# Performance work log

Hardware: AMD Instinct MI355X
Metric: run time of the kernel (lower is better)

The kernel has to match this reference:

```python
import jax, jax.numpy as jnp
import numpy as np

N = 16          # num_transforms
BS = 128        # batch_size
D = 4096        # encoder dim
C, H, W = 3, 64, 64
TEMP = 0.5      # hyperparams.temperature
LAM_H = 1.0     # hyperparams.h
EPS = 1e-8      # torch CosineSimilarity eps


def setup_inputs() -> dict:
    key = jax.random.key(0)
    k1, k2, k3 = jax.random.split(key, 3)
    return {
        "pic_set": jax.random.normal(k1, (N, BS, C, H, W), dtype=jnp.float32),
        "dec_pics": jax.random.normal(k2, (N, BS, C, H, W), dtype=jnp.float32),
        "h": jax.random.normal(k3, (N, BS, D), dtype=jnp.float32),
    }


def _pos_neg_indices(n, bs):
    # Static (numpy) index construction replicating the boolean masks.
    # Positives of row i: all j != i with j % bs == i % bs (sorted, row-major),
    # Negatives of row i: all j with j % bs != i % bs (sorted).
    k = n * bs
    i = np.arange(k)
    cols = (i % bs)[:, None] + np.arange(n)[None, :] * bs          # (K, N)
    pos_idx = cols[cols != i[:, None]].reshape(k, n - 1)            # (K, N-1)
    jj = np.arange(k)
    neg_mask = (jj[None, :] % bs) != (i[:, None] % bs)              # (K, K)
    neg_idx = np.broadcast_to(jj, (k, k))[neg_mask].reshape(k, k - n)  # (K, K-N)
    return jnp.asarray(pos_idx), jnp.asarray(neg_idx)


def _nt_xent(h):
    n, bs, d = h.shape
    k = n * bs
    s = h.reshape(k, d)
    # CosineSimilarity(dim=2) with eps clamp on norms
    nrm = jnp.maximum(jnp.linalg.norm(s, axis=1), EPS)
    sn = s / nrm[:, None]
    simmat = (sn @ sn.T) / TEMP                                     # (K, K)
    pos_idx, neg_idx = _pos_neg_indices(n, bs)
    pos = jnp.take_along_axis(simmat, pos_idx, axis=1)              # (K, N-1)
    neg = jnp.take_along_axis(simmat, neg_idx, axis=1)              # (K, K-N)
    # CrossEntropyLoss(reduction='sum') with label 0 on logits
    # [pos_{i,m}, neg_i] == sum of logsumexp - pos; logsumexp over concat
    # factors as logaddexp(lse(neg_i), pos_{i,m}).
    neg_lse = jax.scipy.special.logsumexp(neg, axis=1)              # (K,)
    loss = jnp.sum(jnp.logaddexp(neg_lse[:, None], pos) - pos)
    kpos = k * (n - 1)
    return loss / kpos


def reference(pic_set, dec_pics, h):
    n, bs = pic_set.shape[0], pic_set.shape[1]
    loss_h = _nt_xent(h)
    # dec_pics[(i+1) % N] cyclic offset, then flat MSE (mean reduction)
    offset = (np.arange(n) + 1) % n
    p = pic_set.reshape(n, bs, -1)
    dshift = dec_pics.reshape(n, bs, -1)[offset]
    loss_pairs = jnp.mean((p - dshift) ** 2)
    return loss_pairs + LAM_H * loss_h
```

## Files before the change

### kernel.cpp

```cpp
#include <hip/hip_runtime.h>
#include <hip/hip_bf16.h>
#include <math.h>

#define N_T   16
#define BSZ   128
#define DDIM  4096
#define KROWS (N_T * BSZ)
#define CHW   (3 * 64 * 64)
#define S_PIC (BSZ * CHW)
#define T_MSE (N_T * S_PIC)
#define KPOS  (KROWS * (N_T - 1))

#define GEMM_BLOCKS 512
#define MSE_BLOCKS  3072

typedef short  bf16x8 __attribute__((ext_vector_type(8)));
typedef float  f32x4  __attribute__((ext_vector_type(4)));

__device__ __forceinline__ float waveReduceSum(float v) {
    for (int off = 32; off > 0; off >>= 1) v += __shfl_down(v, off, 64);
    return v;
}
__device__ __forceinline__ float waveReduceMax(float v) {
    for (int off = 32; off > 0; off >>= 1) v = fmaxf(v, __shfl_down(v, off, 64));
    return v;
}
__device__ __forceinline__ float blockReduceSum(float v) {
    __shared__ float s[8];
    int lane = threadIdx.x & 63, wid = threadIdx.x >> 6;
    v = waveReduceSum(v);
    if (lane == 0) s[wid] = v;
    __syncthreads();
    int nw = (blockDim.x + 63) >> 6;
    v = (threadIdx.x < nw) ? s[threadIdx.x] : 0.0f;
    if (wid == 0) v = waveReduceSum(v);
    return v;
}
__device__ __forceinline__ float blockReduceMax(float v) {
    __shared__ float s[8];
    int lane = threadIdx.x & 63, wid = threadIdx.x >> 6;
    v = waveReduceMax(v);
    if (lane == 0) s[wid] = v;
    __syncthreads();
    int nw = (blockDim.x + 63) >> 6;
    v = (threadIdx.x < nw) ? s[threadIdx.x] : -INFINITY;
    if (wid == 0) v = waveReduceMax(v);
    return v;
}

__device__ __forceinline__ void mse_block(const float* __restrict__ pic,
                                          const float* __restrict__ dec,
                                          float* __restrict__ acc,
                                          int n, int bx) {
    const size_t off = (size_t)n * S_PIC + (size_t)bx * 8192 + threadIdx.x * 4;
    const ptrdiff_t doff = (ptrdiff_t)(((n + 1) & (N_T - 1)) - n) * S_PIC;
    const float* p = pic + off;
    const float* d = pic + off;
    d = dec + off + doff;
    float s0 = 0.f, s1 = 0.f, s2 = 0.f, s3 = 0.f;
#pragma unroll
    for (int k = 0; k < 8; k++) {
        float4 a = *(const float4*)(p + k * 1024);
        float4 b = *(const float4*)(d + k * 1024);
        float dx = a.x - b.x, dy = a.y - b.y, dz = a.z - b.z, dw = a.w - b.w;
        s0 += dx * dx; s1 += dy * dy; s2 += dz * dz; s3 += dw * dw;
    }
    float sum = (s0 + s1) + (s2 + s3);
    sum = blockReduceSum(sum);
    if (threadIdx.x == 0) atomicAdd(acc, sum);
}

__global__ void norm_kernel(const float* __restrict__ h,
                            __hip_bfloat16* __restrict__ hb) {
    const int row = blockIdx.x;
    const float* r = h + (size_t)row * DDIM;
    float ss = 0.0f;
    for (int k = threadIdx.x * 8; k < DDIM; k += blockDim.x * 8) {
        float4 v0 = *(const float4*)(r + k);
        float4 v1 = *(const float4*)(r + k + 4);
        ss += v0.x * v0.x + v0.y * v0.y + v0.z * v0.z + v0.w * v0.w;
        ss += v1.x * v1.x + v1.y * v1.y + v1.z * v1.z + v1.w * v1.w;
    }
    ss = blockReduceSum(ss);
    __shared__ float scale_s;
    if (threadIdx.x == 0) scale_s = 1.0f / fmaxf(sqrtf(ss), 1e-8f);
    __syncthreads();
    const float sc = scale_s;
    __hip_bfloat16* ob = hb + (size_t)row * DDIM;
    for (int k = threadIdx.x * 8; k < DDIM; k += blockDim.x * 8) {
        float4 v0 = *(const float4*)(r + k);
        float4 v1 = *(const float4*)(r + k + 4);
        __hip_bfloat16 t[8];
        t[0] = __float2bfloat16(v0.x * sc); t[1] = __float2bfloat16(v0.y * sc);
        t[2] = __float2bfloat16(v0.z * sc); t[3] = __float2bfloat16(v0.w * sc);
        t[4] = __float2bfloat16(v1.x * sc); t[5] = __float2bfloat16(v1.y * sc);
        t[6] = __float2bfloat16(v1.z * sc); t[7] = __float2bfloat16(v1.w * sc);
        *(bf16x8*)(ob + k) = *(const bf16x8*)t;
    }
}

__global__ __launch_bounds__(256) void mega_kernel(const ushort* __restrict__ X,
                                                   float* __restrict__ Cpart,
                                                   const float* __restrict__ pic,
                                                   const float* __restrict__ dec,
                                                   float* __restrict__ acc) {
    __shared__ ushort As[128 * 32];
    __shared__ ushort Bs[128 * 32];
    const int bid = blockIdx.x;

    if (bid >= GEMM_BLOCKS) {
        const int t = bid - GEMM_BLOCKS;
        mse_block(pic, dec, acc, t & (N_T - 1), t >> 4);
        return;
    }

    const int kz = bid >> 8;
    const int bi = (bid >> 4) & 15, bj = bid & 15;
    const int tid  = threadIdx.x;
    const int wave = tid >> 6, lane = tid & 63;
    const int wm = wave >> 1, wn = wave & 1;
    const int quad = lane >> 4, l16 = lane & 15;

    f32x4 acc_r[4][4];
#pragma unroll
    for (int i = 0; i < 4; i++)
#pragma unroll
        for (int j = 0; j < 4; j++) acc_r[i][j] = (f32x4){0.f, 0.f, 0.f, 0.f};

    const int srow = lane >> 2;
    const int scol = (lane & 3) * 8;
    const ushort* Ag0 = X + (size_t)(bi * 128 + wave * 16       + srow) * DDIM + scol;
    const ushort* Ag1 = X + (size_t)(bi * 128 + (wave + 4) * 16 + srow) * DDIM + scol;
    const ushort* Bg0 = X + (size_t)(bj * 128 + wave * 16       + srow) * DDIM + scol;
    const ushort* Bg1 = X + (size_t)(bj * 128 + (wave + 4) * 16 + srow) * DDIM + scol;
    ushort* Al0 = As + wave * 512;
    ushort* Al1 = As + (wave + 4) * 512;
    ushort* Bl0 = Bs + wave * 512;
    ushort* Bl1 = Bs + (wave + 4) * 512;

    const int k0 = kz * (DDIM / 2), k1 = k0 + (DDIM / 2);
    for (int kk = k0; kk < k1; kk += 32) {
        __syncthreads();
        __builtin_amdgcn_global_load_lds(
            (const __attribute__((address_space(1))) unsigned int*)(Ag0 + kk),
            (__attribute__((address_space(3))) unsigned int*)Al0, 16, 0, 0);
        __builtin_amdgcn_global_load_lds(
            (const __attribute__((address_space(1))) unsigned int*)(Ag1 + kk),
            (__attribute__((address_space(3))) unsigned int*)Al1, 16, 0, 0);
        __builtin_amdgcn_global_load_lds(
            (const __attribute__((address_space(1))) unsigned int*)(Bg0 + kk),
            (__attribute__((address_space(3))) unsigned int*)Bl0, 16, 0, 0);
        __builtin_amdgcn_global_load_lds(
            (const __attribute__((address_space(1))) unsigned int*)(Bg1 + kk),
            (__attribute__((address_space(3))) unsigned int*)Bl1, 16, 0, 0);
        __syncthreads();

        bf16x8 a[4], b[4];
#pragma unroll
        for (int t = 0; t < 4; t++)
            a[t] = *(const bf16x8*)(As + (wm * 64 + t * 16 + l16) * 32 + quad * 8);
#pragma unroll
        for (int t = 0; t < 4; t++)
            b[t] = *(const bf16x8*)(Bs + (wn * 64 + t * 16 + l16) * 32 + quad * 8);
#pragma unroll
        for (int mt = 0; mt < 4; mt++)
#pragma unroll
            for (int nt = 0; nt < 4; nt++)
                acc_r[mt][nt] = __builtin_amdgcn_mfma_f32_16x16x32_bf16(
                    a[mt], b[nt], acc_r[mt][nt], 0, 0, 0);
    }

    float* Cp = Cpart + (size_t)kz * KROWS * KROWS;
#pragma unroll
    for (int mt = 0; mt < 4; mt++) {
#pragma unroll
        for (int r = 0; r < 4; r++) {
            const int row = bi * 128 + wm * 64 + mt * 16 + quad * 4 + r;
            float* o = Cp + (size_t)row * KROWS + bj * 128 + wn * 64 + l16;
#pragma unroll
            for (int nt = 0; nt < 4; nt++) o[nt * 16] = 2.0f * acc_r[mt][nt][r];
        }
    }
}

__global__ __launch_bounds__(256) void mse_kernel(const float* __restrict__ pic,
                                                  const float* __restrict__ dec,
                                                  float* __restrict__ acc) {
    mse_block(pic, dec, acc, blockIdx.y, blockIdx.x);
}

__global__ void lse_kernel(const float* __restrict__ Cpart, float* __restrict__ acc) {
    const int i = blockIdx.x;
    __shared__ float srow[KROWS];
    const float* r0 = Cpart + (size_t)i * KROWS;
    const float* r1 = r0 + (size_t)KROWS * KROWS;
    for (int j = threadIdx.x * 4; j < KROWS; j += blockDim.x * 4) {
        float4 a = *(const float4*)(r0 + j);
        float4 b = *(const float4*)(r1 + j);
        float4 s; s.x = a.x + b.x; s.y = a.y + b.y; s.z = a.z + b.z; s.w = a.w + b.w;
        *(float4*)(srow + j) = s;
    }
    __syncthreads();

    const int ires = i & (BSZ - 1);
    float m = -INFINITY;
    for (int j = threadIdx.x; j < KROWS; j += blockDim.x)
        if ((j & (BSZ - 1)) != ires) m = fmaxf(m, srow[j]);
    m = blockReduceMax(m);
    __shared__ float mS;
    if (threadIdx.x == 0) mS = m;
    __syncthreads();
    m = mS;
    float se = 0.0f;
    for (int j = threadIdx.x; j < KROWS; j += blockDim.x)
        if ((j & (BSZ - 1)) != ires) se += expf(srow[j] - m);
    se = blockReduceSum(se);

    if (threadIdx.x == 0) {
        const float neg_lse = m + logf(se);
        float loss = 0.0f;
#pragma unroll
        for (int t = 0; t < N_T; t++) {
            const int j = ires + t * BSZ;
            if (j == i) continue;
            const float x = neg_lse - srow[j];
            loss += (x > 0.0f) ? (x + log1pf(expf(-x))) : log1pf(expf(x));
        }
        atomicAdd(acc + 1, loss);
    }
}

__global__ void finalize_kernel(const float* __restrict__ acc, float* __restrict__ out) {
    if (threadIdx.x == 0 && blockIdx.x == 0)
        out[0] = acc[0] / (float)T_MSE + acc[1] / (float)KPOS;
}

extern "C" void kernel_launch(void* const* d_in, const int* in_sizes, int n_in,
                              void* d_out, int out_size, void* d_ws, size_t ws_size,
                              hipStream_t stream) {
    const float* pic = (const float*)d_in[0];
    float* dec = (float*)d_in[1];
    const float* h = (const float*)d_in[2];
    float* out = (float*)d_out;

    float* acc = (float*)d_ws;
    const size_t hbuf_bytes   = (size_t)KROWS * DDIM * sizeof(__hip_bfloat16);
    const size_t simmat_bytes = (size_t)2 * KROWS * KROWS * sizeof(float);

    hipMemsetAsync(d_ws, 0, 256, stream);

    if (ws_size >= 256 + hbuf_bytes + simmat_bytes) {
        __hip_bfloat16* hbuf = (__hip_bfloat16*)((char*)d_ws + 256);
        float* simmat = (float*)((char*)d_ws + 256 + hbuf_bytes);
        norm_kernel<<<KROWS, 256, 0, stream>>>(h, hbuf);
        mega_kernel<<<GEMM_BLOCKS + MSE_BLOCKS, 256, 0, stream>>>(
            (const ushort*)hbuf, simmat, pic, dec, acc);
        lse_kernel<<<KROWS, 256, 0, stream>>>(simmat, acc);
    } else {
        __hip_bfloat16* hbuf = (__hip_bfloat16*)dec;
        float* simmat = (float*)((char*)dec + hbuf_bytes);
        mse_kernel<<<dim3(MSE_BLOCKS / N_T, N_T), 256, 0, stream>>>(pic, dec, acc);
        norm_kernel<<<KROWS, 256, 0, stream>>>(h, hbuf);
        mega_kernel<<<GEMM_BLOCKS, 256, 0, stream>>>(
            (const ushort*)hbuf, simmat, pic, dec, acc);
        lse_kernel<<<KROWS, 256, 0, stream>>>(simmat, acc);
    }
    finalize_kernel<<<1, 64, 0, stream>>>(acc, out);
}
```

Baseline: 305.0 us.

## Deepen split-K, swizzle GEMM blocks, drop LSE max pass, fuse finalize

The GEMM k-split depth becomes a template parameter and the default path now splits K four ways instead of two. GEMM block indices are remapped so consecutive blocks spread across k-slices and tiles. The LSE kernel drops its max-reduction pass and uses a fixed shift of 2, which is safe because cosine similarity divided by 0.5 is bounded by 2; it also switches to fast exp and log intrinsics. The memset and finalize launches are removed: accumulator zeroing moves into the norm kernel, and the last LSE block, found through an atomic counter, writes the output. The deeper split doubles the partial-sum memory written and read, which trades extra memory traffic for more GEMM parallelism.

```diff
diff --git a/kernel.cpp b/kernel.cpp
--- a/kernel.cpp
+++ b/kernel.cpp
@@ -11,7 +11,6 @@
 #define T_MSE (N_T * S_PIC)
 #define KPOS  (KROWS * (N_T - 1))
 
-#define GEMM_BLOCKS 512
 #define MSE_BLOCKS  3072
 
 typedef short  bf16x8 __attribute__((ext_vector_type(8)));
@@ -19,10 +18,6 @@
 
 __device__ __forceinline__ float waveReduceSum(float v) {
     for (int off = 32; off > 0; off >>= 1) v += __shfl_down(v, off, 64);
-    return v;
-}
-__device__ __forceinline__ float waveReduceMax(float v) {
-    for (int off = 32; off > 0; off >>= 1) v = fmaxf(v, __shfl_down(v, off, 64));
     return v;
 }
 __device__ __forceinline__ float blockReduceSum(float v) {
@@ -36,17 +31,6 @@
     if (wid == 0) v = waveReduceSum(v);
     return v;
 }
-__device__ __forceinline__ float blockReduceMax(float v) {
-    __shared__ float s[8];
-    int lane = threadIdx.x & 63, wid = threadIdx.x >> 6;
-    v = waveReduceMax(v);
-    if (lane == 0) s[wid] = v;
-    __syncthreads();
-    int nw = (blockDim.x + 63) >> 6;
-    v = (threadIdx.x < nw) ? s[threadIdx.x] : -INFINITY;
-    if (wid == 0) v = waveReduceMax(v);
-    return v;
-}
 
 __device__ __forceinline__ void mse_block(const float* __restrict__ pic,
                                           const float* __restrict__ dec,
@@ -55,8 +39,7 @@
     const size_t off = (size_t)n * S_PIC + (size_t)bx * 8192 + threadIdx.x * 4;
     const ptrdiff_t doff = (ptrdiff_t)(((n + 1) & (N_T - 1)) - n) * S_PIC;
     const float* p = pic + off;
-    const float* d = pic + off;
-    d = dec + off + doff;
+    const float* d = dec + off + doff;
     float s0 = 0.f, s1 = 0.f, s2 = 0.f, s3 = 0.f;
 #pragma unroll
     for (int k = 0; k < 8; k++) {
@@ -71,7 +54,11 @@
 }
 
 __global__ void norm_kernel(const float* __restrict__ h,
-                            __hip_bfloat16* __restrict__ hb) {
+                            __hip_bfloat16* __restrict__ hb,
+                            float* __restrict__ acc, int zero_acc) {
+    if (zero_acc && blockIdx.x == 0 && threadIdx.x < 64)
+        acc[threadIdx.x] = 0.0f;
+
     const int row = blockIdx.x;
     const float* r = h + (size_t)row * DDIM;
     float ss = 0.0f;
@@ -99,6 +86,7 @@
     }
 }
 
+template<int NKZ>
 __global__ __launch_bounds__(256) void mega_kernel(const ushort* __restrict__ X,
                                                    float* __restrict__ Cpart,
                                                    const float* __restrict__ pic,
@@ -106,13 +94,16 @@
                                                    float* __restrict__ acc) {
     __shared__ ushort As[128 * 32];
     __shared__ ushort Bs[128 * 32];
-    const int bid = blockIdx.x;
-
-    if (bid >= GEMM_BLOCKS) {
-        const int t = bid - GEMM_BLOCKS;
+    constexpr int NG = NKZ * 256;
+    int bid = blockIdx.x;
+
+    if (bid >= NG) {
+        const int t = bid - NG;
         mse_block(pic, dec, acc, t & (N_T - 1), t >> 4);
         return;
     }
+
+    bid = (bid & 7) * (NG >> 3) + (bid >> 3);
 
     const int kz = bid >> 8;
     const int bi = (bid >> 4) & 15, bj = bid & 15;
@@ -138,7 +129,8 @@
     ushort* Bl0 = Bs + wave * 512;
     ushort* Bl1 = Bs + (wave + 4) * 512;
 
-    const int k0 = kz * (DDIM / 2), k1 = k0 + (DDIM / 2);
+    constexpr int KS = DDIM / NKZ;
+    const int k0 = kz * KS, k1 = k0 + KS;
     for (int kk = k0; kk < k1; kk += 32) {
         __syncthreads();
         __builtin_amdgcn_global_load_lds(
@@ -189,35 +181,32 @@
     mse_block(pic, dec, acc, blockIdx.y, blockIdx.x);
 }
 
-__global__ void lse_kernel(const float* __restrict__ Cpart, float* __restrict__ acc) {
+template<int NKZ>
+__global__ void lse_kernel(const float* __restrict__ Cpart,
+                           float* __restrict__ acc,
+                           float* __restrict__ out) {
     const int i = blockIdx.x;
     __shared__ float srow[KROWS];
     const float* r0 = Cpart + (size_t)i * KROWS;
-    const float* r1 = r0 + (size_t)KROWS * KROWS;
     for (int j = threadIdx.x * 4; j < KROWS; j += blockDim.x * 4) {
-        float4 a = *(const float4*)(r0 + j);
-        float4 b = *(const float4*)(r1 + j);
-        float4 s; s.x = a.x + b.x; s.y = a.y + b.y; s.z = a.z + b.z; s.w = a.w + b.w;
+        float4 s = *(const float4*)(r0 + j);
+#pragma unroll
+        for (int p = 1; p < NKZ; p++) {
+            float4 b = *(const float4*)(r0 + (size_t)p * KROWS * KROWS + j);
+            s.x += b.x; s.y += b.y; s.z += b.z; s.w += b.w;
+        }
         *(float4*)(srow + j) = s;
     }
     __syncthreads();
 
     const int ires = i & (BSZ - 1);
-    float m = -INFINITY;
-    for (int j = threadIdx.x; j < KROWS; j += blockDim.x)
-        if ((j & (BSZ - 1)) != ires) m = fmaxf(m, srow[j]);
-    m = blockReduceMax(m);
-    __shared__ float mS;
-    if (threadIdx.x == 0) mS = m;
-    __syncthreads();
-    m = mS;
     float se = 0.0f;
     for (int j = threadIdx.x; j < KROWS; j += blockDim.x)
-        if ((j & (BSZ - 1)) != ires) se += expf(srow[j] - m);
+        if ((j & (BSZ - 1)) != ires) se += __expf(srow[j] - 2.0f);
     se = blockReduceSum(se);
 
     if (threadIdx.x == 0) {
-        const float neg_lse = m + logf(se);
+        const float neg_lse = 2.0f + __logf(se);
         float loss = 0.0f;
 #pragma unroll
         for (int t = 0; t < N_T; t++) {
@@ -227,12 +216,14 @@
             loss += (x > 0.0f) ? (x + log1pf(expf(-x))) : log1pf(expf(x));
         }
         atomicAdd(acc + 1, loss);
-    }
-}
-
-__global__ void finalize_kernel(const float* __restrict__ acc, float* __restrict__ out) {
-    if (threadIdx.x == 0 && blockIdx.x == 0)
-        out[0] = acc[0] / (float)T_MSE + acc[1] / (float)KPOS;
+        __threadfence();
+        const int old = atomicAdd((int*)acc + 8, 1);
+        if (old == KROWS - 1) {
+            const float mse = atomicAdd(acc + 0, 0.0f);
+            const float lh  = atomicAdd(acc + 1, 0.0f);
+            out[0] = mse / (float)T_MSE + lh / (float)KPOS;
+        }
+    }
 }
 
 extern "C" void kernel_launch(void* const* d_in, const int* in_sizes, int n_in,
@@ -244,26 +235,31 @@
     float* out = (float*)d_out;
 
     float* acc = (float*)d_ws;
-    const size_t hbuf_bytes   = (size_t)KROWS * DDIM * sizeof(__hip_bfloat16);
-    const size_t simmat_bytes = (size_t)2 * KROWS * KROWS * sizeof(float);
-
-    hipMemsetAsync(d_ws, 0, 256, stream);
-
-    if (ws_size >= 256 + hbuf_bytes + simmat_bytes) {
+    const size_t hbuf_bytes = (size_t)KROWS * DDIM * sizeof(__hip_bfloat16);
+    const size_t part_bytes = (size_t)KROWS * KROWS * sizeof(float);
+
+    if (ws_size >= 256 + hbuf_bytes + 4 * part_bytes) {
         __hip_bfloat16* hbuf = (__hip_bfloat16*)((char*)d_ws + 256);
-        float* simmat = (float*)((char*)d_ws + 256 + hbuf_bytes);
-        norm_kernel<<<KROWS, 256, 0, stream>>>(h, hbuf);
-        mega_kernel<<<GEMM_BLOCKS + MSE_BLOCKS, 256, 0, stream>>>(
-            (const ushort*)hbuf, simmat, pic, dec, acc);
-        lse_kernel<<<KROWS, 256, 0, stream>>>(simmat, acc);
+        float* Cpart = (float*)((char*)d_ws + 256 + hbuf_bytes);
+        norm_kernel<<<KROWS, 256, 0, stream>>>(h, hbuf, acc, 1);
+        mega_kernel<4><<<4 * 256 + MSE_BLOCKS, 256, 0, stream>>>(
+            (const ushort*)hbuf, Cpart, pic, dec, acc);
+        lse_kernel<4><<<KROWS, 256, 0, stream>>>(Cpart, acc, out);
+    } else if (ws_size >= 256 + hbuf_bytes + 2 * part_bytes) {
+        __hip_bfloat16* hbuf = (__hip_bfloat16*)((char*)d_ws + 256);
+        float* Cpart = (float*)((char*)d_ws + 256 + hbuf_bytes);
+        norm_kernel<<<KROWS, 256, 0, stream>>>(h, hbuf, acc, 1);
+        mega_kernel<2><<<2 * 256 + MSE_BLOCKS, 256, 0, stream>>>(
+            (const ushort*)hbuf, Cpart, pic, dec, acc);
+        lse_kernel<2><<<KROWS, 256, 0, stream>>>(Cpart, acc, out);
     } else {
+        hipMemsetAsync(d_ws, 0, 256, stream);
         __hip_bfloat16* hbuf = (__hip_bfloat16*)dec;
-        float* simmat = (float*)((char*)dec + hbuf_bytes);
+        float* Cpart = (float*)((char*)dec + hbuf_bytes);
         mse_kernel<<<dim3(MSE_BLOCKS / N_T, N_T), 256, 0, stream>>>(pic, dec, acc);
-        norm_kernel<<<KROWS, 256, 0, stream>>>(h, hbuf);
-        mega_kernel<<<GEMM_BLOCKS, 256, 0, stream>>>(
-            (const ushort*)hbuf, simmat, pic, dec, acc);
-        lse_kernel<<<KROWS, 256, 0, stream>>>(simmat, acc);
-    }
-    finalize_kernel<<<1, 64, 0, stream>>>(acc, out);
-}
+        norm_kernel<<<KROWS, 256, 0, stream>>>(h, hbuf, acc, 0);
+        mega_kernel<2><<<2 * 256, 256, 0, stream>>>(
+            (const ushort*)hbuf, Cpart, pic, dec, acc);
+        lse_kernel<2><<<KROWS, 256, 0, stream>>>(Cpart, acc, out);
+    }
+}
```

After: 345.2 us. +13.2%, slower.
